# Optimization experiments

Hardware: AMD Instinct MI355X
Metric: run time of the kernel (lower is better)

Reference implementation:

```python
import jax, jax.numpy as jnp
import numpy as np

BITS = 4
QMAX = 2 ** (BITS - 1) - 1   # 7
OFF = 2 ** (BITS - 1)        # 8
L = 2 ** BITS                # 16 LUT levels per operand


def _quant(x):
    """Symmetric per-tensor quantization to signed BITS-bit levels.
    Returns integer-valued levels (as float, in [-OFF, QMAX]) and the scale."""
    s = jnp.maximum(jnp.max(jnp.abs(x)) / QMAX, 1e-8)
    q = jnp.clip(jnp.round(x / s), -OFF, QMAX)
    return q, s


def _lut_conv3x3(x, w, b, lut):
    """3x3 same-padding conv where every scalar multiply a*w is replaced by
    lut[idx(a), idx(w)]. x:[B,C,H,W], w:[O,C,3,3], b:[O], lut:[L,L]."""
    B, C, H, W = x.shape
    O = w.shape[0]
    qx, sx = _quant(x)
    qw, sw = _quant(w)
    # zero-padding: level 0 is the quantized value 0, so padding is exact
    xp = jnp.pad(qx, ((0, 0), (0, 0), (1, 1), (1, 1)))
    # im2col: [B, C, 9, H, W] -> [B, H, W, K], K = C*9 (order: c-major, then kh,kw)
    patches = jnp.stack([xp[:, :, i:i + H, j:j + W]
                         for i in range(3) for j in range(3)], axis=2)
    K = C * 9
    patches = patches.reshape(B, K, H, W).transpose(0, 2, 3, 1)
    idx_a = (patches + OFF).astype(jnp.int32)            # [B,H,W,K]
    mapped = lut[idx_a]                                   # [B,H,W,K,L]
    idx_w = (qw.reshape(O, K).T + OFF).astype(jnp.int32)  # [K,O]
    onehot_w = jax.nn.one_hot(idx_w, L, dtype=x.dtype)    # [K,O,L]
    # out[b,o,h,w] = sum_k lut[idx_a[b,h,w,k], idx_w[k,o]]
    out = jnp.einsum('bhwkl,kol->bohw', mapped, onehot_w)
    return out * (sx * sw) + b[None, :, None, None]


def _lut_linear(x, w, b, lut):
    """x:[B,F], w:[O,F], b:[O], lut:[L,L]; y[b,o]=sum_f lut[idx(x),idx(w)]."""
    qx, sx = _quant(x)
    qw, sw = _quant(w)
    idx_a = (qx + OFF).astype(jnp.int32)                 # [B,F]
    mapped = lut[idx_a]                                   # [B,F,L]
    idx_w = (qw.T + OFF).astype(jnp.int32)                # [F,O]
    onehot_w = jax.nn.one_hot(idx_w, L, dtype=x.dtype)    # [F,O,L]
    out = jnp.einsum('bfl,fol->bo', mapped, onehot_w)
    return out * (sx * sw) + b[None, :]


def _maxpool2(x):
    B, C, H, W = x.shape
    return x.reshape(B, C, H // 2, 2, W // 2, 2).max(axis=(3, 5))


def setup_inputs() -> dict:
    key = jax.random.key(0)
    ks = jax.random.split(key, 20)
    d = {}
    d['x'] = jax.random.normal(ks[0], (8, 3, 32, 32), jnp.float32)
    conv_shapes = [(64, 3), (192, 64), (384, 192), (256, 384), (256, 256)]
    for i, (o, c) in enumerate(conv_shapes):
        d[f'w{i}'] = jax.random.normal(ks[1 + 2 * i], (o, c, 3, 3), jnp.float32) * 0.05
        d[f'b{i}'] = jax.random.normal(ks[2 + 2 * i], (o,), jnp.float32) * 0.01
    fc_shapes = [(4096, 4096), (4096, 4096), (10, 4096)]
    for j, (o, f) in enumerate(fc_shapes):
        d[f'w{5 + j}'] = jax.random.normal(ks[11 + 2 * j], (o, f), jnp.float32) * 0.02
        d[f'b{5 + j}'] = jax.random.normal(ks[12 + 2 * j], (o,), jnp.float32) * 0.01
    # per-layer approximate-multiplier LUTs: exact product of signed levels + error
    levels = jnp.arange(-OFF, OFF, dtype=jnp.float32)       # [-8..7]
    base = jnp.outer(levels, levels)                        # [16,16]
    noise = jax.random.normal(ks[17], (8, L, L), jnp.float32) * 0.25
    d['luts'] = base[None, :, :] + noise
    return d


def reference(x, w0, b0, w1, b1, w2, b2, w3, b3, w4, b4,
              w5, b5, w6, b6, w7, b7, luts):
    relu = jax.nn.relu
    h = relu(_lut_conv3x3(x, w0, b0, luts[0]))
    h = _maxpool2(h)                                  # [B,64,16,16]
    h = relu(_lut_conv3x3(h, w1, b1, luts[1]))
    h = _maxpool2(h)                                  # [B,192,8,8]
    h = relu(_lut_conv3x3(h, w2, b2, luts[2]))        # [B,384,8,8]
    h = relu(_lut_conv3x3(h, w3, b3, luts[3]))        # [B,256,8,8]
    h = relu(_lut_conv3x3(h, w4, b4, luts[4]))
    h = _maxpool2(h)                                  # [B,256,4,4]
    h = h.reshape(h.shape[0], 256 * 4 * 4)
    h = relu(_lut_linear(h, w5, b5, luts[5]))         # dropout = identity (eval)
    h = relu(_lut_linear(h, w6, b6, luts[6]))
    return _lut_linear(h, w7, b7, luts[7])            # [B,10]
```

## Files before the change

### kernel.cpp

```cpp
#include <hip/hip_runtime.h>
#include <stdint.h>


#define DI __device__ __forceinline__

constexpr size_t alup(size_t x){ return (x + 511) & ~(size_t)511; }
constexpr size_t O_SLOTS = 0;
constexpr size_t O_IA0 = 512;
constexpr size_t O_IA5 = alup(O_IA0 + 24576);
constexpr size_t O_IA6 = alup(O_IA5 + 32768);
constexpr size_t O_IA7 = alup(O_IA6 + 32768);
constexpr size_t O_WP0 = alup(O_IA7 + 32768);
constexpr size_t O_WP1 = alup(O_WP0 + 864);
constexpr size_t O_WP2 = alup(O_WP1 + 55296);
constexpr size_t O_WP3 = alup(O_WP2 + 331776);
constexpr size_t O_WP4 = alup(O_WP3 + 442368);
constexpr size_t O_A1  = alup(O_WP4 + 294912);
constexpr size_t O_A2  = alup(O_A1 + 1048576);
constexpr size_t O_A3  = alup(O_A2 + 786432);
constexpr size_t O_A4  = alup(O_A3 + 1572864);
constexpr size_t O_A5  = alup(O_A4 + 1048576);
constexpr size_t O_H5  = alup(O_A5 + 262144);
constexpr size_t O_H6  = alup(O_H5 + 262144);
constexpr size_t O_P1  = alup(O_H6 + 262144);
constexpr size_t O_P2  = O_P1 + 3145728;
constexpr size_t O_P3  = O_P2 + 1572864;
constexpr size_t O_P4  = O_P3 + 1048576;
constexpr int    PZ_D4 = 212992;


DI double getscale(const double* slots, int i){ return fmax(slots[i] / 7.0, 1e-8); }
DI int quant_idx_r(double v, double r){
  double q = fmin(fmax(rint(v * r), -8.0), 7.0);
  return (int)q + 8;
}
DI void atomicMaxD(double* addr, double v){
  atomicMax((unsigned long long*)addr, (unsigned long long)__double_as_longlong(v));
}

__global__ __launch_bounds__(256) void k_zero_all(double4* pz, double* slots){
  int i = blockIdx.x*256 + threadIdx.x;
  if (i < PZ_D4){ double4 z; z.x=z.y=z.z=z.w=0.0; pz[i] = z; }
  else if (i - PZ_D4 < 16) slots[i - PZ_D4] = 0.0;
}

__global__ __launch_bounds__(256) void k_wmax(
    const float* w0, const float* w1, const float* w2, const float* w3, const float* w4,
    const float* w5, const float* w6, const float* w7, const float* x, double* slots)
{
  const int sizes[9] = {1728,110592,663552,884736,589824,16777216,16777216,40960,24576};
  const int cum[10]  = {0,1,5,26,53,71,583,1095,1097,1098};
  int bid = blockIdx.x;
  int seg = 0;
  #pragma unroll
  for (int s2 = 0; s2 < 9; ++s2) if (bid >= cum[s2+1]) seg = s2+1;
  const float* p;
  switch (seg){
    case 0: p = w0; break; case 1: p = w1; break; case 2: p = w2; break;
    case 3: p = w3; break; case 4: p = w4; break; case 5: p = w5; break;
    case 6: p = w6; break; case 7: p = w7; break; default: p = x; break;
  }
  int n = sizes[seg];
  long base = (long)(bid - cum[seg]) * 32768;
  float m = 0.f;
  for (long i = base + threadIdx.x * 4; i < base + 32768 && i < (long)n; i += 1024){
    float4 v = *(const float4*)(p + i);
    m = fmaxf(m, fmaxf(fmaxf(fabsf(v.x), fabsf(v.y)), fmaxf(fabsf(v.z), fabsf(v.w))));
  }
  #pragma unroll
  for (int off = 32; off; off >>= 1) m = fmaxf(m, __shfl_xor(m, off, 64));
  __shared__ float red[4];
  if ((threadIdx.x & 63) == 0) red[threadIdx.x >> 6] = m;
  __syncthreads();
  if (threadIdx.x == 0)
    atomicMaxD(&slots[seg], (double)fmaxf(fmaxf(red[0], red[1]), fmaxf(red[2], red[3])));
}

__global__ __launch_bounds__(256) void k_wq(
    const float* w0, const float* w1, const float* w2, const float* w3, const float* w4,
    const float* x, const double* slots, uint8_t* ws)
{
  int item = blockIdx.x * 256 + threadIdx.x;
  if (item < 281304){
    const float* w; uint32_t* wp; int K; int r; double s;
    if (item < 216)        { w=w0; wp=(uint32_t*)(ws+O_WP0); K=27;   r=item;        s=getscale(slots,0); }
    else if (item < 14040) { w=w1; wp=(uint32_t*)(ws+O_WP1); K=576;  r=item-216;    s=getscale(slots,1); }
    else if (item < 96984) { w=w2; wp=(uint32_t*)(ws+O_WP2); K=1728; r=item-14040;  s=getscale(slots,2); }
    else if (item < 207576){ w=w3; wp=(uint32_t*)(ws+O_WP3); K=3456; r=item-96984;  s=getscale(slots,3); }
    else                   { w=w4; wp=(uint32_t*)(ws+O_WP4); K=2304; r=item-207576; s=getscale(slots,4); }
    double rs = 1.0 / s;
    int og = r / K, k = r % K;
    uint32_t pack = 0;
    #pragma unroll
    for (int j = 0; j < 8; ++j){
      double wv = (double)w[(size_t)(og*8 + j)*K + k];
      pack |= (uint32_t)quant_idx_r(wv, rs) << (4*j);
    }
    wp[og*K + k] = pack;
  } else if (item < 287448){
    int i2 = item - 281304;
    double rs = 1.0 / getscale(slots, 8);
    uint32_t pack = 0;
    #pragma unroll
    for (int r2 = 0; r2 < 4; ++r2)
      pack |= (uint32_t)quant_idx_r((double)x[i2*4 + r2], rs) << (8*r2);
    ((uint32_t*)(ws + O_IA0))[i2] = pack;
  }
}

__global__ __launch_bounds__(1024) void k_conv0(
    const uint8_t* __restrict__ ia0, const uint32_t* __restrict__ wp0,
    const float* __restrict__ lut_g, const float* __restrict__ bias,
    double* slots, double* __restrict__ a1)
{
  __shared__ double lutT[256];
  __shared__ uint8_t acts[3*34*34];
  __shared__ double red[16];
  int tid = threadIdx.x;
  if (tid < 256) lutT[(tid & 15)*16 + (tid >> 4)] = (double)lut_g[tid];
  int b = blockIdx.x >> 6, o = blockIdx.x & 63;
  for (int i = tid; i < 3*34*34; i += 1024){
    int c = i / 1156, r = (i / 34) % 34, cc = i % 34;
    int y = r - 1, x2 = cc - 1;
    uint8_t v = 8;
    if (y >= 0 && y < 32 && x2 >= 0 && x2 < 32)
      v = ia0[((b*3 + c)*32 + y)*32 + x2];
    acts[i] = v;
  }
  __syncthreads();
  int y = tid >> 5, x2 = tid & 31;
  double scale = getscale(slots, 8) * getscale(slots, 0);
  double bo = (double)bias[o];
  double sum = 0.0;
  #pragma unroll
  for (int c = 0; c < 3; ++c)
    #pragma unroll
    for (int ty = 0; ty < 3; ++ty)
      #pragma unroll
      for (int tx = 0; tx < 3; ++tx){
        int ia = acts[c*1156 + (y + ty)*34 + (x2 + tx)];
        uint32_t sw = wp0[(o >> 3)*27 + c*9 + ty*3 + tx];
        int iw = (sw >> ((o & 7)*4)) & 15;
        sum += lutT[iw*16 + ia];
      }
  double h = fmax(sum*scale + bo, 0.0);
  double p = fmax(h, __shfl_xor(h, 1, 64));
  p = fmax(p, __shfl_xor(p, 32, 64));
  if (!(x2 & 1) && !(y & 1))
    a1[((b*64 + o)*16 + (y >> 1))*16 + (x2 >> 1)] = p;
  double m = h;
  #pragma unroll
  for (int off = 32; off; off >>= 1) m = fmax(m, __shfl_xor(m, off, 64));
  if ((tid & 63) == 0) red[tid >> 6] = m;
  __syncthreads();
  if (tid == 0){
    double mm = red[0];
    #pragma unroll
    for (int w2 = 1; w2 < 16; ++w2) mm = fmax(mm, red[w2]);
    atomicMaxD(&slots[9], mm);
  }
}

template<int C, int O, int H, int W, int CT, int ROWS, int SP, int KS>
__global__ __launch_bounds__(256, 8) void k_conv(
    const double* __restrict__ ain, const uint32_t* __restrict__ wp,
    const float* __restrict__ lut_g, const double* __restrict__ slots,
    int sx_slot, double* __restrict__ P)
{
  constexpr int KT = CT*9;
  constexpr int AW = W + 2, AH = ROWS + 2;
  __shared__ double lutT[256];
  __shared__ alignas(16) uint32_t wps[4*CT*12];
  __shared__ uint8_t acts[CT*AH*AW];
  int tid = threadIdx.x;
  int bx = blockIdx.x;
  int ks = bx % KS; int rem = bx / KS;
  int ob = rem % (O/32); rem /= (O/32);
  int sp = rem % SP; int b = rem / SP;
  lutT[(tid & 15)*16 + (tid >> 4)] = (double)lut_g[tid];
  for (int i = tid; i < 4*KT; i += 256){
    int w2 = i / KT, k = i % KT;
    wps[(w2*CT + k/9)*12 + (k%9)] = wp[(size_t)(ob*4 + w2)*(C*9) + (size_t)ks*KT + k];
  }
  double rsx = 1.0 / getscale(slots, sx_slot);
  for (int i = tid; i < CT*AH*AW; i += 256){
    int ct = i / (AH*AW);
    int r  = (i / AW) % AH;
    int cc = i % AW;
    int y = sp*ROWS + r - 1, x2 = cc - 1;
    int v = 8;
    if (y >= 0 && y < H && x2 >= 0 && x2 < W)
      v = quant_idx_r(ain[(((size_t)b*C + ks*CT + ct)*H + y)*W + x2], rsx);
    acts[i] = (uint8_t)(v << 3);
  }
  __syncthreads();
  int wid = tid >> 6, lane = tid & 63;
  int ly = lane / W, lx = lane % W;
  double acc[8] = {0,0,0,0,0,0,0,0};
  const char* lutB = (const char*)lutT;
  #pragma unroll 1
  for (int ct = 0; ct < CT; ++ct){
    int abase = (ct*AH + ly)*AW + lx;
    const uint32_t* wr2 = &wps[(wid*CT + ct)*12];
    uint4 wa = *(const uint4*)(wr2);
    uint4 wb = *(const uint4*)(wr2 + 4);
    uint32_t wc = wr2[8];
    uint32_t wv[9] = {wa.x, wa.y, wa.z, wa.w, wb.x, wb.y, wb.z, wb.w, wc};
    uint32_t sw[9];
    #pragma unroll
    for (int t = 0; t < 9; ++t)
      sw[t] = (uint32_t)__builtin_amdgcn_readfirstlane((int)wv[t]);
    uint32_t ia8[9];
    #pragma unroll
    for (int t = 0; t < 9; ++t)
      ia8[t] = acts[abase + (t/3)*AW + (t%3)];
    #pragma unroll
    for (int j = 0; j < 8; ++j){
      double tv[9];
      #pragma unroll
      for (int t = 0; t < 9; ++t)
        tv[t] = *(const double*)(lutB + (((sw[t] >> (4*j)) & 15u) << 7) + ia8[t]);
      #pragma unroll
      for (int t = 0; t < 9; ++t) acc[j] += tv[t];
    }
  }
  int y = sp*ROWS + ly;
  int obase = ob*32 + wid*8;
  #pragma unroll
  for (int j = 0; j < 8; ++j)
    atomicAdd(&P[(((size_t)b*O + obase + j)*H + y)*W + lx], acc[j]);
}

template<int O, int Hc, int Wc, bool POOL>
__global__ __launch_bounds__(256) void k_post(
    const double* __restrict__ P, const float* __restrict__ bias,
    double* __restrict__ aout, double* slots, int sx_slot, int sw_slot, int ma_slot)
{
  constexpr int Ho = POOL ? Hc/2 : Hc, Wo = POOL ? Wc/2 : Wc;
  int i = blockIdx.x*256 + threadIdx.x;
  int x2 = i % Wo, y = (i / Wo) % Ho, o = (i / (Wo*Ho)) % O, b = i / (Wo*Ho*O);
  double scale = getscale(slots, sx_slot) * getscale(slots, sw_slot);
  double bo = (double)bias[o];
  double res;
  if (POOL){
    double p = 0.0;
    #pragma unroll
    for (int dy = 0; dy < 2; ++dy)
    #pragma unroll
    for (int dx = 0; dx < 2; ++dx){
      double s = P[(((size_t)b*O + o)*Hc + y*2+dy)*Wc + x2*2+dx];
      p = fmax(p, fmax(s*scale + bo, 0.0));
    }
    res = p;
  } else {
    double s = P[(((size_t)b*O + o)*Hc + y)*Wc + x2];
    res = fmax(s*scale + bo, 0.0);
  }
  aout[i] = res;
  double m = res;
  #pragma unroll
  for (int off = 32; off; off >>= 1) m = fmax(m, __shfl_xor(m, off, 64));
  __shared__ double red[4];
  if ((threadIdx.x & 63) == 0) red[threadIdx.x >> 6] = m;
  __syncthreads();
  if (threadIdx.x == 0)
    atomicMaxD(&slots[ma_slot], fmax(fmax(red[0],red[1]), fmax(red[2],red[3])));
}

__global__ __launch_bounds__(256) void k_aq_fc(
    const double* __restrict__ in, uint2* __restrict__ lh,
    const double* slots, int slot)
{
  int f = blockIdx.x*256 + threadIdx.x;
  double rs = 1.0 / getscale(slots, slot);
  uint32_t l = 0, h = 0;
  #pragma unroll
  for (int b2 = 0; b2 < 4; ++b2)
    l |= (uint32_t)(quant_idx_r(in[(size_t)b2*4096 + f], rs) << 2) << (8*b2);
  #pragma unroll
  for (int b2 = 4; b2 < 8; ++b2)
    h |= (uint32_t)(quant_idx_r(in[(size_t)b2*4096 + f], rs) << 2) << (8*(b2-4));
  lh[f] = make_uint2(l, h);
}

template<bool RELU>
__global__ __launch_bounds__(256) void k_fc(
    const float* __restrict__ Wm, const float* __restrict__ bias,
    const uint2* __restrict__ lh_g, const float* __restrict__ lut_g,
    double* __restrict__ out, double* slots, int sx_slot, int sw_slot, int ma_slot)
{
  __shared__ float lutT[256];
  __shared__ uint2 lhs[4096];
  __shared__ double red[4];
  int tid = threadIdx.x;
  lutT[(tid & 15)*16 + (tid >> 4)] = lut_g[tid];
  for (int i = tid; i < 4096; i += 256) lhs[i] = lh_g[i];
  __syncthreads();
  double sw = getscale(slots, sw_slot);
  double rsw = 1.0 / sw;
  double scale = getscale(slots, sx_slot) * sw;
  int wid = tid >> 6, lane = tid & 63;
  int o = blockIdx.x*4 + wid;
  const float* wr = Wm + (size_t)o*4096;
  double acc[8] = {0,0,0,0,0,0,0,0};
  #pragma unroll 2
  for (int ch = 0; ch < 64; ++ch){
    int f = ch*64 + lane;
    unsigned iw = (unsigned)quant_idx_r((double)wr[f], rsw);
    const char* lb = (const char*)lutT + (iw << 6);
    uint2 lh = lhs[f];
    acc[0] += (double)*(const float*)(lb + (lh.x & 255u));
    acc[1] += (double)*(const float*)(lb + ((lh.x >> 8) & 255u));
    acc[2] += (double)*(const float*)(lb + ((lh.x >> 16) & 255u));
    acc[3] += (double)*(const float*)(lb + (lh.x >> 24));
    acc[4] += (double)*(const float*)(lb + (lh.y & 255u));
    acc[5] += (double)*(const float*)(lb + ((lh.y >> 8) & 255u));
    acc[6] += (double)*(const float*)(lb + ((lh.y >> 16) & 255u));
    acc[7] += (double)*(const float*)(lb + (lh.y >> 24));
  }
  #pragma unroll
  for (int off = 32; off; off >>= 1)
    #pragma unroll
    for (int b2 = 0; b2 < 8; ++b2) acc[b2] += __shfl_xor(acc[b2], off, 64);
  if (lane == 0){
    double m = 0.0;
    double bo = (double)bias[o];
    #pragma unroll
    for (int b2 = 0; b2 < 8; ++b2){
      double h = acc[b2]*scale + bo;
      if (RELU) h = fmax(h, 0.0);
      out[(size_t)b2*4096 + o] = h;
      m = fmax(m, fabs(h));
    }
    red[wid] = m;
  }
  __syncthreads();
  if (tid == 0)
    atomicMaxD(&slots[ma_slot], fmax(fmax(red[0],red[1]), fmax(red[2],red[3])));
}

__global__ __launch_bounds__(1024) void k_fc7(
    const float* __restrict__ Wm, const float* __restrict__ bias,
    const uint2* __restrict__ lh_g, const float* __restrict__ lut_g,
    float* __restrict__ out, const double* slots)
{
  __shared__ float lutT[256];
  __shared__ uint2 lhs[4096];
  __shared__ double red[16][8];
  int tid = threadIdx.x;
  if (tid < 256) lutT[(tid & 15)*16 + (tid >> 4)] = lut_g[tid];
  for (int i = tid; i < 4096; i += 1024) lhs[i] = lh_g[i];
  __syncthreads();
  double sw = getscale(slots, 7);
  double rsw = 1.0 / sw;
  double scale = getscale(slots, 15) * sw;
  int o = blockIdx.x;
  const float* wr = Wm + (size_t)o*4096;
  double acc[8] = {0,0,0,0,0,0,0,0};
  #pragma unroll
  for (int ch = 0; ch < 4; ++ch){
    int f = ch*1024 + tid;
    unsigned iw = (unsigned)quant_idx_r((double)wr[f], rsw);
    const char* lb = (const char*)lutT + (iw << 6);
    uint2 lh = lhs[f];
    acc[0] += (double)*(const float*)(lb + (lh.x & 255u));
    acc[1] += (double)*(const float*)(lb + ((lh.x >> 8) & 255u));
    acc[2] += (double)*(const float*)(lb + ((lh.x >> 16) & 255u));
    acc[3] += (double)*(const float*)(lb + (lh.x >> 24));
    acc[4] += (double)*(const float*)(lb + (lh.y & 255u));
    acc[5] += (double)*(const float*)(lb + ((lh.y >> 8) & 255u));
    acc[6] += (double)*(const float*)(lb + ((lh.y >> 16) & 255u));
    acc[7] += (double)*(const float*)(lb + (lh.y >> 24));
  }
  int wid = tid >> 6, lane = tid & 63;
  #pragma unroll
  for (int off = 32; off; off >>= 1)
    #pragma unroll
    for (int b2 = 0; b2 < 8; ++b2) acc[b2] += __shfl_xor(acc[b2], off, 64);
  if (lane == 0){
    #pragma unroll
    for (int b2 = 0; b2 < 8; ++b2) red[wid][b2] = acc[b2];
  }
  __syncthreads();
  if (tid < 8){
    double v = 0.0;
    #pragma unroll
    for (int w2 = 0; w2 < 16; ++w2) v += red[w2][tid];
    out[tid*10 + o] = (float)(v*scale + (double)bias[o]);
  }
}

extern "C" void kernel_launch(void* const* d_in, const int* in_sizes, int n_in,
                              void* d_out, int out_size, void* d_ws, size_t ws_size,
                              hipStream_t stream)
{
  (void)in_sizes; (void)n_in; (void)out_size; (void)ws_size;
  const float* x  = (const float*)d_in[0];
  const float* w0 = (const float*)d_in[1];  const float* b0 = (const float*)d_in[2];
  const float* w1 = (const float*)d_in[3];  const float* b1 = (const float*)d_in[4];
  const float* w2 = (const float*)d_in[5];  const float* b2 = (const float*)d_in[6];
  const float* w3 = (const float*)d_in[7];  const float* b3 = (const float*)d_in[8];
  const float* w4 = (const float*)d_in[9];  const float* b4 = (const float*)d_in[10];
  const float* w5 = (const float*)d_in[11]; const float* b5 = (const float*)d_in[12];
  const float* w6 = (const float*)d_in[13]; const float* b6 = (const float*)d_in[14];
  const float* w7 = (const float*)d_in[15]; const float* b7 = (const float*)d_in[16];
  const float* luts = (const float*)d_in[17];

  uint8_t* ws = (uint8_t*)d_ws;
  double* slots = (double*)(ws + O_SLOTS);
  const uint8_t* IA0 = ws + O_IA0;
  uint2 *IA5 = (uint2*)(ws + O_IA5), *IA6 = (uint2*)(ws + O_IA6), *IA7 = (uint2*)(ws + O_IA7);
  const uint32_t* WP0 = (const uint32_t*)(ws + O_WP0);
  const uint32_t* WP1 = (const uint32_t*)(ws + O_WP1);
  const uint32_t* WP2 = (const uint32_t*)(ws + O_WP2);
  const uint32_t* WP3 = (const uint32_t*)(ws + O_WP3);
  const uint32_t* WP4 = (const uint32_t*)(ws + O_WP4);
  double *A1 = (double*)(ws + O_A1), *A2 = (double*)(ws + O_A2), *A3 = (double*)(ws + O_A3);
  double *A4 = (double*)(ws + O_A4), *A5 = (double*)(ws + O_A5);
  double *H5 = (double*)(ws + O_H5), *H6 = (double*)(ws + O_H6);
  double *P1 = (double*)(ws + O_P1), *P2 = (double*)(ws + O_P2);
  double *P3 = (double*)(ws + O_P3), *P4 = (double*)(ws + O_P4);

  k_zero_all<<<833, 256, 0, stream>>>((double4*)(ws + O_P1), slots);
  k_wmax<<<1098, 256, 0, stream>>>(w0,w1,w2,w3,w4,w5,w6,w7,x,slots);
  k_wq<<<1123, 256, 0, stream>>>(w0,w1,w2,w3,w4,x,slots,ws);

  k_conv0<<<512, 1024, 0, stream>>>(IA0, WP0, luts + 0, b0, slots, A1);

  k_conv<64,192,16,16,8,4,4,8><<<1536, 256, 0, stream>>>(A1, WP1, luts + 256, slots, 9, P1);
  k_post<192,16,16,true><<<384, 256, 0, stream>>>(P1, b1, A2, slots, 9, 1, 10);

  k_conv<192,384,8,8,12,8,1,16><<<1536, 256, 0, stream>>>(A2, WP2, luts + 512, slots, 10, P2);
  k_post<384,8,8,false><<<768, 256, 0, stream>>>(P2, b2, A3, slots, 10, 2, 11);

  k_conv<384,256,8,8,12,8,1,32><<<2048, 256, 0, stream>>>(A3, WP3, luts + 768, slots, 11, P3);
  k_post<256,8,8,false><<<512, 256, 0, stream>>>(P3, b3, A4, slots, 11, 3, 12);

  k_conv<256,256,8,8,8,8,1,32><<<2048, 256, 0, stream>>>(A4, WP4, luts + 1024, slots, 12, P4);
  k_post<256,8,8,true><<<128, 256, 0, stream>>>(P4, b4, A5, slots, 12, 4, 13);
  k_aq_fc<<<16, 256, 0, stream>>>(A5, IA5, slots, 13);

  k_fc<true><<<1024, 256, 0, stream>>>(w5, b5, IA5, luts + 1280, H5, slots, 13, 5, 14);
  k_aq_fc<<<16, 256, 0, stream>>>(H5, IA6, slots, 14);
  k_fc<true><<<1024, 256, 0, stream>>>(w6, b6, IA6, luts + 1536, H6, slots, 14, 6, 15);
  k_aq_fc<<<16, 256, 0, stream>>>(H6, IA7, slots, 15);
  k_fc7<<<10, 1024, 0, stream>>>(w7, b7, IA7, luts + 1792, (float*)d_out, slots);
}
```

Baseline: 470.1 us.

## Split conv input channels across waves with in-block reduction; unroll weight max scan

```diff
diff --git a/kernel.cpp b/kernel.cpp
--- a/kernel.cpp
+++ b/kernel.cpp
@@ -44,6 +44,10 @@
   else if (i - PZ_D4 < 16) slots[i - PZ_D4] = 0.0;
 }
 
+DI float fmax4(float4 v){
+  return fmaxf(fmaxf(fabsf(v.x), fabsf(v.y)), fmaxf(fabsf(v.z), fabsf(v.w)));
+}
+
 __global__ __launch_bounds__(256) void k_wmax(
     const float* w0, const float* w1, const float* w2, const float* w3, const float* w4,
     const float* w5, const float* w6, const float* w7, const float* x, double* slots)
@@ -60,13 +64,21 @@
     case 3: p = w3; break; case 4: p = w4; break; case 5: p = w5; break;
     case 6: p = w6; break; case 7: p = w7; break; default: p = x; break;
   }
-  int n = sizes[seg];
+  long n = sizes[seg];
   long base = (long)(bid - cum[seg]) * 32768;
-  float m = 0.f;
-  for (long i = base + threadIdx.x * 4; i < base + 32768 && i < (long)n; i += 1024){
-    float4 v = *(const float4*)(p + i);
-    m = fmaxf(m, fmaxf(fmaxf(fabsf(v.x), fabsf(v.y)), fmaxf(fabsf(v.z), fabsf(v.w))));
-  }
+  long lim = n < base + 32768 ? n : base + 32768;
+  long i = base + threadIdx.x * 4;
+  float m0 = 0.f, m1 = 0.f, m2 = 0.f, m3 = 0.f;
+  for (; i + 3076 <= lim; i += 4096){
+    float4 v0 = *(const float4*)(p + i);
+    float4 v1 = *(const float4*)(p + i + 1024);
+    float4 v2 = *(const float4*)(p + i + 2048);
+    float4 v3 = *(const float4*)(p + i + 3072);
+    m0 = fmaxf(m0, fmax4(v0)); m1 = fmaxf(m1, fmax4(v1));
+    m2 = fmaxf(m2, fmax4(v2)); m3 = fmaxf(m3, fmax4(v3));
+  }
+  for (; i < lim; i += 1024) m0 = fmaxf(m0, fmax4(*(const float4*)(p + i)));
+  float m = fmaxf(fmaxf(m0, m1), fmaxf(m2, m3));
   #pragma unroll
   for (int off = 32; off; off >>= 1) m = fmaxf(m, __shfl_xor(m, off, 64));
   __shared__ float red[4];
@@ -161,36 +173,37 @@
   }
 }
 
-template<int C, int O, int H, int W, int CT, int ROWS, int SP, int KS>
-__global__ __launch_bounds__(256, 8) void k_conv(
+template<int C, int O, int H, int W, int CTW, int ROWS, int SP, int KSO>
+__global__ __launch_bounds__(256, 6) void k_conv(
     const double* __restrict__ ain, const uint32_t* __restrict__ wp,
     const float* __restrict__ lut_g, const double* __restrict__ slots,
     int sx_slot, double* __restrict__ P)
 {
-  constexpr int KT = CT*9;
+  constexpr int CTB = CTW*4;
   constexpr int AW = W + 2, AH = ROWS + 2;
   __shared__ double lutT[256];
-  __shared__ alignas(16) uint32_t wps[4*CT*12];
-  __shared__ uint8_t acts[CT*AH*AW];
+  __shared__ alignas(16) uint32_t wps[CTB*12];
+  __shared__ uint8_t acts[CTB*AH*AW];
+  __shared__ double redb[3*8*64];
   int tid = threadIdx.x;
   int bx = blockIdx.x;
-  int ks = bx % KS; int rem = bx / KS;
-  int ob = rem % (O/32); rem /= (O/32);
+  int ks = bx % KSO; int rem = bx / KSO;
+  int ob = rem % (O/8); rem /= (O/8);
   int sp = rem % SP; int b = rem / SP;
   lutT[(tid & 15)*16 + (tid >> 4)] = (double)lut_g[tid];
-  for (int i = tid; i < 4*KT; i += 256){
-    int w2 = i / KT, k = i % KT;
-    wps[(w2*CT + k/9)*12 + (k%9)] = wp[(size_t)(ob*4 + w2)*(C*9) + (size_t)ks*KT + k];
+  for (int i = tid; i < CTB*9; i += 256){
+    int ct = i / 9, k = i % 9;
+    wps[ct*12 + k] = wp[(size_t)ob*(C*9) + (size_t)(ks*CTB + ct)*9 + k];
   }
   double rsx = 1.0 / getscale(slots, sx_slot);
-  for (int i = tid; i < CT*AH*AW; i += 256){
+  for (int i = tid; i < CTB*AH*AW; i += 256){
     int ct = i / (AH*AW);
     int r  = (i / AW) % AH;
     int cc = i % AW;
     int y = sp*ROWS + r - 1, x2 = cc - 1;
     int v = 8;
     if (y >= 0 && y < H && x2 >= 0 && x2 < W)
-      v = quant_idx_r(ain[(((size_t)b*C + ks*CT + ct)*H + y)*W + x2], rsx);
+      v = quant_idx_r(ain[(((size_t)b*C + ks*CTB + ct)*H + y)*W + x2], rsx);
     acts[i] = (uint8_t)(v << 3);
   }
   __syncthreads();
@@ -199,9 +212,10 @@
   double acc[8] = {0,0,0,0,0,0,0,0};
   const char* lutB = (const char*)lutT;
   #pragma unroll 1
-  for (int ct = 0; ct < CT; ++ct){
-    int abase = (ct*AH + ly)*AW + lx;
-    const uint32_t* wr2 = &wps[(wid*CT + ct)*12];
+  for (int ct = 0; ct < CTW; ++ct){
+    int ctg = wid*CTW + ct;
+    int abase = (ctg*AH + ly)*AW + lx;
+    const uint32_t* wr2 = &wps[ctg*12];
     uint4 wa = *(const uint4*)(wr2);
     uint4 wb = *(const uint4*)(wr2 + 4);
     uint32_t wc = wr2[8];
@@ -224,11 +238,21 @@
       for (int t = 0; t < 9; ++t) acc[j] += tv[t];
     }
   }
-  int y = sp*ROWS + ly;
-  int obase = ob*32 + wid*8;
-  #pragma unroll
-  for (int j = 0; j < 8; ++j)
-    atomicAdd(&P[(((size_t)b*O + obase + j)*H + y)*W + lx], acc[j]);
+  if (wid){
+    #pragma unroll
+    for (int j = 0; j < 8; ++j) redb[((wid-1)*8 + j)*64 + lane] = acc[j];
+  }
+  __syncthreads();
+  if (wid == 0){
+    #pragma unroll
+    for (int w2 = 0; w2 < 3; ++w2)
+      #pragma unroll
+      for (int j = 0; j < 8; ++j) acc[j] += redb[(w2*8 + j)*64 + lane];
+    int y = sp*ROWS + ly;
+    #pragma unroll
+    for (int j = 0; j < 8; ++j)
+      atomicAdd(&P[(((size_t)b*O + ob*8 + j)*H + y)*W + lx], acc[j]);
+  }
 }
 
 template<int O, int Hc, int Wc, bool POOL>
@@ -427,16 +451,16 @@
 
   k_conv0<<<512, 1024, 0, stream>>>(IA0, WP0, luts + 0, b0, slots, A1);
 
-  k_conv<64,192,16,16,8,4,4,8><<<1536, 256, 0, stream>>>(A1, WP1, luts + 256, slots, 9, P1);
+  k_conv<64,192,16,16,8,4,4,2><<<1536, 256, 0, stream>>>(A1, WP1, luts + 256, slots, 9, P1);
   k_post<192,16,16,true><<<384, 256, 0, stream>>>(P1, b1, A2, slots, 9, 1, 10);
 
-  k_conv<192,384,8,8,12,8,1,16><<<1536, 256, 0, stream>>>(A2, WP2, luts + 512, slots, 10, P2);
+  k_conv<192,384,8,8,12,8,1,4><<<1536, 256, 0, stream>>>(A2, WP2, luts + 512, slots, 10, P2);
   k_post<384,8,8,false><<<768, 256, 0, stream>>>(P2, b2, A3, slots, 10, 2, 11);
 
-  k_conv<384,256,8,8,12,8,1,32><<<2048, 256, 0, stream>>>(A3, WP3, luts + 768, slots, 11, P3);
+  k_conv<384,256,8,8,12,8,1,8><<<2048, 256, 0, stream>>>(A3, WP3, luts + 768, slots, 11, P3);
   k_post<256,8,8,false><<<512, 256, 0, stream>>>(P3, b3, A4, slots, 11, 3, 12);
 
-  k_conv<256,256,8,8,8,8,1,32><<<2048, 256, 0, stream>>>(A4, WP4, luts + 1024, slots, 12, P4);
+  k_conv<256,256,8,8,8,8,1,8><<<2048, 256, 0, stream>>>(A4, WP4, luts + 1024, slots, 12, P4);
   k_post<256,8,8,true><<<128, 256, 0, stream>>>(P4, b4, A5, slots, 12, 4, 13);
   k_aq_fc<<<16, 256, 0, stream>>>(A5, IA5, slots, 13);
 
```

Measured after the change: 505.9 us. 7.6% more time.

## Use paired-output double2 LUT in conv3/conv4 and unroll weight max reduction

Applied to the files above, without the earlier changes.

```diff
diff --git a/kernel.cpp b/kernel.cpp
--- a/kernel.cpp
+++ b/kernel.cpp
@@ -44,6 +44,10 @@
   else if (i - PZ_D4 < 16) slots[i - PZ_D4] = 0.0;
 }
 
+DI float fmax4(float4 v){
+  return fmaxf(fmaxf(fabsf(v.x), fabsf(v.y)), fmaxf(fabsf(v.z), fabsf(v.w)));
+}
+
 __global__ __launch_bounds__(256) void k_wmax(
     const float* w0, const float* w1, const float* w2, const float* w3, const float* w4,
     const float* w5, const float* w6, const float* w7, const float* x, double* slots)
@@ -60,13 +64,21 @@
     case 3: p = w3; break; case 4: p = w4; break; case 5: p = w5; break;
     case 6: p = w6; break; case 7: p = w7; break; default: p = x; break;
   }
-  int n = sizes[seg];
+  long n = sizes[seg];
   long base = (long)(bid - cum[seg]) * 32768;
-  float m = 0.f;
-  for (long i = base + threadIdx.x * 4; i < base + 32768 && i < (long)n; i += 1024){
-    float4 v = *(const float4*)(p + i);
-    m = fmaxf(m, fmaxf(fmaxf(fabsf(v.x), fabsf(v.y)), fmaxf(fabsf(v.z), fabsf(v.w))));
-  }
+  long lim = n < base + 32768 ? n : base + 32768;
+  long i = base + threadIdx.x * 4;
+  float m0 = 0.f, m1 = 0.f, m2 = 0.f, m3 = 0.f;
+  for (; i + 3076 <= lim; i += 4096){
+    float4 v0 = *(const float4*)(p + i);
+    float4 v1 = *(const float4*)(p + i + 1024);
+    float4 v2 = *(const float4*)(p + i + 2048);
+    float4 v3 = *(const float4*)(p + i + 3072);
+    m0 = fmaxf(m0, fmax4(v0)); m1 = fmaxf(m1, fmax4(v1));
+    m2 = fmaxf(m2, fmax4(v2)); m3 = fmaxf(m3, fmax4(v3));
+  }
+  for (; i < lim; i += 1024) m0 = fmaxf(m0, fmax4(*(const float4*)(p + i)));
+  float m = fmaxf(fmaxf(m0, m1), fmaxf(m2, m3));
   #pragma unroll
   for (int off = 32; off; off >>= 1) m = fmaxf(m, __shfl_xor(m, off, 64));
   __shared__ float red[4];
@@ -222,6 +234,83 @@
         tv[t] = *(const double*)(lutB + (((sw[t] >> (4*j)) & 15u) << 7) + ia8[t]);
       #pragma unroll
       for (int t = 0; t < 9; ++t) acc[j] += tv[t];
+    }
+  }
+  int y = sp*ROWS + ly;
+  int obase = ob*32 + wid*8;
+  #pragma unroll
+  for (int j = 0; j < 8; ++j)
+    atomicAdd(&P[(((size_t)b*O + obase + j)*H + y)*W + lx], acc[j]);
+}
+
+template<int C, int O, int H, int W, int CT, int ROWS, int SP, int KS>
+__global__ __launch_bounds__(256, 2) void k_convP(
+    const double* __restrict__ ain, const uint32_t* __restrict__ wp,
+    const float* __restrict__ lut_g, const double* __restrict__ slots,
+    int sx_slot, double* __restrict__ P)
+{
+  constexpr int KT = CT*9;
+  constexpr int AW = W + 2, AH = ROWS + 2;
+  __shared__ double2 lutP[4096];
+  __shared__ alignas(16) uint32_t wps[4*CT*12];
+  __shared__ uint8_t acts[CT*AH*AW];
+  int tid = threadIdx.x;
+  int bx = blockIdx.x;
+  int ks = bx % KS; int rem = bx / KS;
+  int ob = rem % (O/32); rem /= (O/32);
+  int sp = rem % SP; int b = rem / SP;
+  for (int i = tid; i < 4096; i += 256){
+    int pr = i >> 4, ia = i & 15;
+    lutP[i] = make_double2((double)lut_g[ia*16 + (pr & 15)],
+                           (double)lut_g[ia*16 + (pr >> 4)]);
+  }
+  for (int i = tid; i < 4*KT; i += 256){
+    int w2 = i / KT, k = i % KT;
+    wps[(w2*CT + k/9)*12 + (k%9)] = wp[(size_t)(ob*4 + w2)*(C*9) + (size_t)ks*KT + k];
+  }
+  double rsx = 1.0 / getscale(slots, sx_slot);
+  for (int i = tid; i < CT*AH*AW; i += 256){
+    int ct = i / (AH*AW);
+    int r  = (i / AW) % AH;
+    int cc = i % AW;
+    int y = sp*ROWS + r - 1, x2 = cc - 1;
+    int v = 8;
+    if (y >= 0 && y < H && x2 >= 0 && x2 < W)
+      v = quant_idx_r(ain[(((size_t)b*C + ks*CT + ct)*H + y)*W + x2], rsx);
+    acts[i] = (uint8_t)(v << 4);
+  }
+  __syncthreads();
+  int wid = tid >> 6, lane = tid & 63;
+  int ly = lane / W, lx = lane % W;
+  double acc[8] = {0,0,0,0,0,0,0,0};
+  const char* lutB = (const char*)lutP;
+  #pragma unroll 1
+  for (int ct = 0; ct < CT; ++ct){
+    int abase = (ct*AH + ly)*AW + lx;
+    const uint32_t* wr2 = &wps[(wid*CT + ct)*12];
+    uint4 wa = *(const uint4*)(wr2);
+    uint4 wb = *(const uint4*)(wr2 + 4);
+    uint32_t wc = wr2[8];
+    uint32_t wv[9] = {wa.x, wa.y, wa.z, wa.w, wb.x, wb.y, wb.z, wb.w, wc};
+    uint32_t sw[9];
+    #pragma unroll
+    for (int t = 0; t < 9; ++t)
+      sw[t] = (uint32_t)__builtin_amdgcn_readfirstlane((int)wv[t]);
+    uint32_t ia16[9];
+    #pragma unroll
+    for (int t = 0; t < 9; ++t)
+      ia16[t] = acts[abase + (t/3)*AW + (t%3)];
+    #pragma unroll
+    for (int bj = 0; bj < 4; ++bj){
+      double2 tv[9];
+      #pragma unroll
+      for (int t = 0; t < 9; ++t)
+        tv[t] = *(const double2*)(lutB + (((sw[t] >> (8*bj)) & 255u) << 8) + ia16[t]);
+      #pragma unroll
+      for (int t = 0; t < 9; ++t){
+        acc[2*bj]   += tv[t].x;
+        acc[2*bj+1] += tv[t].y;
+      }
     }
   }
   int y = sp*ROWS + ly;
@@ -433,10 +522,10 @@
   k_conv<192,384,8,8,12,8,1,16><<<1536, 256, 0, stream>>>(A2, WP2, luts + 512, slots, 10, P2);
   k_post<384,8,8,false><<<768, 256, 0, stream>>>(P2, b2, A3, slots, 10, 2, 11);
 
-  k_conv<384,256,8,8,12,8,1,32><<<2048, 256, 0, stream>>>(A3, WP3, luts + 768, slots, 11, P3);
+  k_convP<384,256,8,8,12,8,1,32><<<2048, 256, 0, stream>>>(A3, WP3, luts + 768, slots, 11, P3);
   k_post<256,8,8,false><<<512, 256, 0, stream>>>(P3, b3, A4, slots, 11, 3, 12);
 
-  k_conv<256,256,8,8,8,8,1,32><<<2048, 256, 0, stream>>>(A4, WP4, luts + 1024, slots, 12, P4);
+  k_convP<256,256,8,8,8,8,1,32><<<2048, 256, 0, stream>>>(A4, WP4, luts + 1024, slots, 12, P4);
   k_post<256,8,8,true><<<128, 256, 0, stream>>>(P4, b4, A5, slots, 12, 4, 13);
   k_aq_fc<<<16, 256, 0, stream>>>(A5, IA5, slots, 13);
 
```

Result: slower. 537.5 us (+14.3%).
